# Optimization experiments

Measured on AMD Instinct MI355X. Metric: run time of the kernel, lower is better.

## Reference

```python
import jax, jax.numpy as jnp
import numpy as np

N = 256
MAX_LENGTH = 1024
BATCH = 32768


def _transition(n):
    # HiPPO-LegS transition matrices (float64 numpy, matches torch module)
    q = np.arange(n, dtype=np.float64)
    col, row = np.meshgrid(q, q)
    r = 2 * q + 1
    M = -(np.where(row >= col, r, 0) - np.diag(q))
    T = np.sqrt(np.diag(2 * q + 1))
    A = T @ M @ np.linalg.inv(T)
    B = np.diag(T)  # squeezed (N,)
    return A, B


def _build_stacked(n, max_length):
    # Bilinear (Tustin) discretization at every timescale t=1..max_length.
    A, B = _transition(n)
    ts = np.arange(1, max_length + 1, dtype=np.float64)  # (L,)
    At = A[None] / ts[:, None, None]                     # (L,N,N)
    Bt = B[None] / ts[:, None]                           # (L,N)
    I = np.eye(n)
    lhs = I[None] - At / 2                               # (L,N,N), lower triangular
    A_stacked = np.linalg.solve(lhs, I[None] + At / 2)   # (L,N,N)
    B_stacked = np.linalg.solve(lhs, Bt[..., None])[..., 0]  # (L,N)
    return A_stacked.astype(np.float32), B_stacked.astype(np.float32)


def setup_inputs() -> dict:
    key = jax.random.key(0)
    k1, k2 = jax.random.split(key)
    A_np, B_np = _build_stacked(N, MAX_LENGTH)
    return {
        "c": jax.random.normal(k1, (BATCH, N), dtype=jnp.float32),
        "f": jax.random.normal(k2, (BATCH, 1), dtype=jnp.float32),
        "A_stacked": jnp.asarray(A_np),  # (L, N, N) buffer
        "B_stacked": jnp.asarray(B_np),  # (L, N) buffer
        "t": 512,
    }


def reference(c, f, A_stacked, B_stacked, t):
    # F.linear(c, A) == c @ A.T ; then scaled add of new value f
    A = A_stacked[t]            # (N, N)
    b = B_stacked[t]            # (N,)
    return c @ A.T + b * f      # (BATCH, N)
```

## Files before the change

### kernel.cpp

```cpp
#include <hip/hip_runtime.h>
#include <cstdint>
#include <cstddef>

typedef _Float16 half8 __attribute__((ext_vector_type(8)));
typedef float f32x4 __attribute__((ext_vector_type(4)));

static constexpr int kN  = 256;
static constexpr int kBM = 64;
static constexpr size_t kLDS = 72 * 1024;

__device__ __constant__ const int kBase[16] =
    {0, 1, 2, 4, 6, 9, 12, 16, 20, 25, 30, 36, 42, 49, 56, 64};

__global__ __launch_bounds__(256) void hippo_prep(
    const float* __restrict__ A_stacked, const int* __restrict__ tptr,
    _Float16* __restrict__ a16)
{
    const int t = tptr[0];
    const float* __restrict__ A = A_stacked + (size_t)t * kN * kN;
    const int tid = blockIdx.x * 256 + threadIdx.x;
    const int ksh = tid >> 12;
    const int nt  = (tid >> 8) & 15;
    const int ks2 = (tid >> 6) & 3;
    const int l   = tid & 63;
    const int row = nt * 16 + (l & 15);
    const int k0  = (ksh * 4 + ks2) * 32 + ((l >> 4) << 3);
    const float* __restrict__ src = A + (size_t)row * kN + k0;
    f32x4 v0 = *(const f32x4*)(src);
    f32x4 v1 = *(const f32x4*)(src + 4);
    half8 h;
    h[0] = (_Float16)v0[0]; h[1] = (_Float16)v0[1];
    h[2] = (_Float16)v0[2]; h[3] = (_Float16)v0[3];
    h[4] = (_Float16)v1[0]; h[5] = (_Float16)v1[1];
    h[6] = (_Float16)v1[2]; h[7] = (_Float16)v1[3];
    ((half8*)a16)[tid] = h;
}

__global__ __launch_bounds__(256, 2) void hippo_gemm(
    const float* __restrict__ c, const float* __restrict__ f,
    const float* __restrict__ Bst, const int* __restrict__ tptr,
    const _Float16* __restrict__ a16, float* __restrict__ out)
{
    extern __shared__ char lds_raw[];

    const int tid  = threadIdx.x;
    const int l    = tid & 63;
    const int wid  = tid >> 6;
    const int lo16 = l & 15;
    const int hi4  = l >> 4;
    const int bid  = blockIdx.x;
    const int m0   = bid * kBM + wid * 16;

    const char* __restrict__ gsrc = (const char*)a16;
    #pragma unroll
    for (int j = 0; j < 4; ++j) {
        const int nt   = wid + j * 4;
        const int kmax = nt >> 1;
        #pragma unroll
        for (int ks = 0; ks < 8; ++ks) {
            if (ks <= kmax) {
                const size_t soff =
                    (size_t)(((ks >> 2) * 16 + nt) * 4 + (ks & 3)) * 1024 + (size_t)l * 16;
                const size_t doff = (size_t)(kBase[nt] + ks) * 1024 + (size_t)l * 16;
                __builtin_amdgcn_global_load_lds(
                    (const __attribute__((address_space(1))) void*)(gsrc + soff),
                    (__attribute__((address_space(3))) void*)(lds_raw + doff),
                    16, 0, 0);
            }
        }
    }

    const float* __restrict__ cptr = c + (size_t)(m0 + lo16) * kN + (hi4 << 3);
    f32x4 cv0[4], cv1[4];
    #pragma unroll
    for (int ks = 0; ks < 4; ++ks) {
        cv0[ks] = *(const f32x4*)(cptr + 128 + ks * 32);
        cv1[ks] = *(const f32x4*)(cptr + 128 + ks * 32 + 4);
    }

    const int t = tptr[0];
    const float* __restrict__ brow = Bst + (size_t)t * kN;
    float bvs[16];
    #pragma unroll
    for (int nt = 0; nt < 16; ++nt) bvs[nt] = brow[nt * 16 + lo16];
    float fv[4];
    #pragma unroll
    for (int r = 0; r < 4; ++r) fv[r] = f[m0 + (hi4 << 2) + r];

    __syncthreads();

    half8 af[4];
    #pragma unroll
    for (int ks = 0; ks < 4; ++ks) {
        af[ks][0] = (_Float16)cv0[ks][0]; af[ks][1] = (_Float16)cv0[ks][1];
        af[ks][2] = (_Float16)cv0[ks][2]; af[ks][3] = (_Float16)cv0[ks][3];
        af[ks][4] = (_Float16)cv1[ks][0]; af[ks][5] = (_Float16)cv1[ks][1];
        af[ks][6] = (_Float16)cv1[ks][2]; af[ks][7] = (_Float16)cv1[ks][3];
    }

    f32x4 dv0[4], dv1[4];
    #pragma unroll
    for (int ks = 0; ks < 4; ++ks) {
        dv0[ks] = *(const f32x4*)(cptr + ks * 32);
        dv1[ks] = *(const f32x4*)(cptr + ks * 32 + 4);
    }

    const half8* __restrict__ Bs = (const half8*)lds_raw;
    f32x4 acc[16];
    #pragma unroll
    for (int i = 0; i < 16; ++i) acc[i] = (f32x4){0.f, 0.f, 0.f, 0.f};
    #pragma unroll
    for (int ks2 = 0; ks2 < 4; ++ks2) {
        #pragma unroll
        for (int nt = 0; nt < 16; ++nt) {
            if (nt >= 8 + 2 * ks2) {
                half8 bf = Bs[(kBase[nt] + 4 + ks2) * 64 + l];
                acc[nt] = __builtin_amdgcn_mfma_f32_16x16x32_f16(af[ks2], bf, acc[nt], 0, 0, 0);
            }
        }
    }

    half8 ag[4];
    #pragma unroll
    for (int ks = 0; ks < 4; ++ks) {
        ag[ks][0] = (_Float16)dv0[ks][0]; ag[ks][1] = (_Float16)dv0[ks][1];
        ag[ks][2] = (_Float16)dv0[ks][2]; ag[ks][3] = (_Float16)dv0[ks][3];
        ag[ks][4] = (_Float16)dv1[ks][0]; ag[ks][5] = (_Float16)dv1[ks][1];
        ag[ks][6] = (_Float16)dv1[ks][2]; ag[ks][7] = (_Float16)dv1[ks][3];
    }

    float* __restrict__ obase = out + (size_t)(m0 + (hi4 << 2)) * kN + lo16;
    #pragma unroll
    for (int nt = 0; nt < 16; ++nt) {
        f32x4 a = acc[nt];
        #pragma unroll
        for (int ks2 = 0; ks2 < 4; ++ks2) {
            if (ks2 <= (nt >> 1)) {
                half8 bf = Bs[(kBase[nt] + ks2) * 64 + l];
                a = __builtin_amdgcn_mfma_f32_16x16x32_f16(ag[ks2], bf, a, 0, 0, 0);
            }
        }
        #pragma unroll
        for (int r = 0; r < 4; ++r)
            obase[(size_t)r * kN + nt * 16] = a[r] + bvs[nt] * fv[r];
    }
}

extern "C" void kernel_launch(void* const* d_in, const int* in_sizes, int n_in,
                              void* d_out, int out_size, void* d_ws, size_t ws_size,
                              hipStream_t stream) {
    const float* c   = (const float*)d_in[0];
    const float* f   = (const float*)d_in[1];
    const float* A   = (const float*)d_in[2];
    const float* B   = (const float*)d_in[3];
    const int*   t   = (const int*)d_in[4];
    float* out = (float*)d_out;
    _Float16* a16 = (_Float16*)d_ws;

    const int batch = in_sizes[0] / kN;

    hipFuncSetAttribute((const void*)hippo_gemm,
                        hipFuncAttributeMaxDynamicSharedMemorySize,
                        (int)kLDS);

    hipLaunchKernelGGL(hippo_prep, dim3(32), dim3(256), 0, stream, A, t, a16);
    hipLaunchKernelGGL(hippo_gemm, dim3(batch / kBM), dim3(256), kLDS, stream,
                       c, f, B, t, a16, out);
}
```

Before: 22.44 us.

## Split output columns across two wave groups with 512-thread blocks

Doubles the block to 512 threads so each of four row-waves is paired with a second wave. The pair splits the 16 output column tiles by parity, which halves the accumulator registers per wave and raises the number of waves available to hide memory latency. The LDS fill of the triangular A tiles is rewritten as a flat table-driven copy spread evenly over all 8 waves. The cost is that each c row tile is loaded and converted twice, once by each wave of the pair, and the 72KB LDS per block may limit how many blocks fit on a CU.

```diff
diff --git a/kernel.cpp b/kernel.cpp
--- a/kernel.cpp
+++ b/kernel.cpp
@@ -11,6 +11,12 @@
 
 __device__ __constant__ const int kBase[16] =
     {0, 1, 2, 4, 6, 9, 12, 16, 20, 25, 30, 36, 42, 49, 56, 64};
+__device__ __constant__ const int kSrc[72] = {
+    0, 4, 8, 9, 12, 13, 16, 17, 18, 20, 21, 22, 24, 25, 26, 27,
+    28, 29, 30, 31, 32, 33, 34, 35, 96, 36, 37, 38, 39, 100, 40, 41,
+    42, 43, 104, 105, 44, 45, 46, 47, 108, 109, 48, 49, 50, 51, 112, 113,
+    114, 52, 53, 54, 55, 116, 117, 118, 56, 57, 58, 59, 120, 121, 122, 123,
+    60, 61, 62, 63, 124, 125, 126, 127};
 
 __global__ __launch_bounds__(256) void hippo_prep(
     const float* __restrict__ A_stacked, const int* __restrict__ tptr,
@@ -36,7 +42,7 @@
     ((half8*)a16)[tid] = h;
 }
 
-__global__ __launch_bounds__(256, 2) void hippo_gemm(
+__global__ __launch_bounds__(512, 4) void hippo_gemm(
     const float* __restrict__ c, const float* __restrict__ f,
     const float* __restrict__ Bst, const int* __restrict__ tptr,
     const _Float16* __restrict__ a16, float* __restrict__ out)
@@ -46,28 +52,23 @@
     const int tid  = threadIdx.x;
     const int l    = tid & 63;
     const int wid  = tid >> 6;
+    const int wm   = wid & 3;
+    const int wp   = wid >> 2;
     const int lo16 = l & 15;
     const int hi4  = l >> 4;
     const int bid  = blockIdx.x;
-    const int m0   = bid * kBM + wid * 16;
+    const int m0   = bid * kBM + wm * 16;
 
     const char* __restrict__ gsrc = (const char*)a16;
     #pragma unroll
-    for (int j = 0; j < 4; ++j) {
-        const int nt   = wid + j * 4;
-        const int kmax = nt >> 1;
-        #pragma unroll
-        for (int ks = 0; ks < 8; ++ks) {
-            if (ks <= kmax) {
-                const size_t soff =
-                    (size_t)(((ks >> 2) * 16 + nt) * 4 + (ks & 3)) * 1024 + (size_t)l * 16;
-                const size_t doff = (size_t)(kBase[nt] + ks) * 1024 + (size_t)l * 16;
-                __builtin_amdgcn_global_load_lds(
-                    (const __attribute__((address_space(1))) void*)(gsrc + soff),
-                    (__attribute__((address_space(3))) void*)(lds_raw + doff),
-                    16, 0, 0);
-            }
-        }
+    for (int i = 0; i < 9; ++i) {
+        const int ci = i * 8 + wid;
+        const size_t soff = (size_t)kSrc[ci] * 1024 + (size_t)l * 16;
+        const size_t doff = (size_t)ci * 1024 + (size_t)l * 16;
+        __builtin_amdgcn_global_load_lds(
+            (const __attribute__((address_space(1))) void*)(gsrc + soff),
+            (__attribute__((address_space(3))) void*)(lds_raw + doff),
+            16, 0, 0);
     }
 
     const float* __restrict__ cptr = c + (size_t)(m0 + lo16) * kN + (hi4 << 3);
@@ -80,9 +81,9 @@
 
     const int t = tptr[0];
     const float* __restrict__ brow = Bst + (size_t)t * kN;
-    float bvs[16];
+    float bvs[8];
     #pragma unroll
-    for (int nt = 0; nt < 16; ++nt) bvs[nt] = brow[nt * 16 + lo16];
+    for (int j = 0; j < 8; ++j) bvs[j] = brow[(wp + 2 * j) * 16 + lo16];
     float fv[4];
     #pragma unroll
     for (int r = 0; r < 4; ++r) fv[r] = f[m0 + (hi4 << 2) + r];
@@ -106,16 +107,17 @@
     }
 
     const half8* __restrict__ Bs = (const half8*)lds_raw;
-    f32x4 acc[16];
+    f32x4 acc[8];
     #pragma unroll
-    for (int i = 0; i < 16; ++i) acc[i] = (f32x4){0.f, 0.f, 0.f, 0.f};
+    for (int i = 0; i < 8; ++i) acc[i] = (f32x4){0.f, 0.f, 0.f, 0.f};
     #pragma unroll
     for (int ks2 = 0; ks2 < 4; ++ks2) {
         #pragma unroll
-        for (int nt = 0; nt < 16; ++nt) {
+        for (int j = 0; j < 8; ++j) {
+            const int nt = wp + 2 * j;
             if (nt >= 8 + 2 * ks2) {
                 half8 bf = Bs[(kBase[nt] + 4 + ks2) * 64 + l];
-                acc[nt] = __builtin_amdgcn_mfma_f32_16x16x32_f16(af[ks2], bf, acc[nt], 0, 0, 0);
+                acc[j] = __builtin_amdgcn_mfma_f32_16x16x32_f16(af[ks2], bf, acc[j], 0, 0, 0);
             }
         }
     }
@@ -131,8 +133,9 @@
 
     float* __restrict__ obase = out + (size_t)(m0 + (hi4 << 2)) * kN + lo16;
     #pragma unroll
-    for (int nt = 0; nt < 16; ++nt) {
-        f32x4 a = acc[nt];
+    for (int j = 0; j < 8; ++j) {
+        const int nt = wp + 2 * j;
+        f32x4 a = acc[j];
         #pragma unroll
         for (int ks2 = 0; ks2 < 4; ++ks2) {
             if (ks2 <= (nt >> 1)) {
@@ -142,7 +145,7 @@
         }
         #pragma unroll
         for (int r = 0; r < 4; ++r)
-            obase[(size_t)r * kN + nt * 16] = a[r] + bvs[nt] * fv[r];
+            obase[(size_t)r * kN + nt * 16] = a[r] + bvs[j] * fv[r];
     }
 }
 
@@ -164,6 +167,6 @@
                         (int)kLDS);
 
     hipLaunchKernelGGL(hippo_prep, dim3(32), dim3(256), 0, stream, A, t, a16);
-    hipLaunchKernelGGL(hippo_gemm, dim3(batch / kBM), dim3(256), kLDS, stream,
+    hipLaunchKernelGGL(hippo_gemm, dim3(batch / kBM), dim3(512), kLDS, stream,
                        c, f, B, t, a16, out);
 }
```

Result: slower. 26.55 us (+18.3%).
